# Optimization experiments

Hardware: AMD Instinct MI355X
Metric: run time of the kernel (lower is better)

Reference implementation:

```python
import jax, jax.numpy as jnp
import numpy as np

N, E, D, S, H, L = 20000, 320000, 128, 16, 4, 64


def _ln(x, g, b):
    m = x.mean(-1, keepdims=True)
    v = jnp.mean((x - m) ** 2, -1, keepdims=True)
    return (x - m) / jnp.sqrt(v + 1e-6) * g + b


def _mlp3(x, w1, b1, g1, be1, w2, b2, g2, be2, w3, b3):
    h = jax.nn.silu(_ln(x @ w1 + b1, g1, be1))
    h = jax.nn.silu(_ln(h @ w2 + b2, g2, be2))
    return h @ w3 + b3


def _seg_softmax(a, idx, n):
    # torch_geometric.utils.softmax: per-destination-group stable softmax
    m = jax.ops.segment_max(a, idx, num_segments=n)
    m = jnp.where(jnp.isfinite(m), m, 0.0)
    e = jnp.exp(a - m[idx])
    s = jax.ops.segment_sum(e, idx, num_segments=n)
    return e / (s[idx] + 1e-16)


def setup_inputs() -> dict:
    key = jax.random.key(0)
    ks = jax.random.split(key, 32)
    rn = lambda k, sh, sc=1.0: jax.random.normal(k, sh, dtype=jnp.float32) * sc
    li = lambda k, fi, fo: rn(k, (fi, fo), 1.0 / np.sqrt(fi))
    z = lambda n_: jnp.zeros((n_,), jnp.float32)
    o = lambda n_: jnp.ones((n_,), jnp.float32)
    inp = {
        'node_in': rn(ks[0], (N, D)),
        'node_embed': rn(ks[1], (N, D)),
        'edge_sh': rn(ks[2], (E, S)),
        'edge_length_embedding': rn(ks[3], (E, L)),
        'edge_src': jax.random.randint(ks[4], (E,), 0, N, dtype=jnp.int32),
        'edge_dst': jax.random.randint(ks[5], (E,), 0, N, dtype=jnp.int32),
        'batch': jnp.zeros((N,), jnp.int32),
        'pre_lin_w': li(ks[6], 2 * D + L, D),
        'tp2_w1': li(ks[7], L, 64), 'tp2_b1': z(64),
        'tp2_w2': li(ks[8], 64, H * S), 'tp2_b2': z(H * S),
        'a_w1': li(ks[9], L, 64), 'a_b1': z(64), 'a_g1': o(64), 'a_be1': z(64),
        'a_w2': li(ks[10], 64, 64), 'a_b2': z(64), 'a_g2': o(64), 'a_be2': z(64),
        'a_w3': li(ks[11], 64, H), 'a_b3': z(H),
        'lin_w': li(ks[12], D * H, D),
        'lin_edge_w': li(ks[13], D * H, 64),
        's_w1': li(ks[14], 64, 64), 's_b1': z(64), 's_g1': o(64), 's_be1': z(64),
        's_w2': li(ks[15], 64, 64), 's_b2': z(64), 's_g2': o(64), 's_be2': z(64),
        's_w3': li(ks[16], 64, 32), 's_b3': z(32),
    }
    return inp


def reference(node_in, node_embed, edge_sh, edge_length_embedding, edge_src, edge_dst, batch,
              pre_lin_w, tp2_w1, tp2_b1, tp2_w2, tp2_b2,
              a_w1, a_b1, a_g1, a_be1, a_w2, a_b2, a_g2, a_be2, a_w3, a_b3,
              lin_w, lin_edge_w,
              s_w1, s_b1, s_g1, s_be1, s_w2, s_b2, s_g2, s_be2, s_w3, s_b3):
    e = edge_length_embedding.shape[0]
    n = node_in.shape[0]
    # gather + pre_lin
    msg = jnp.concatenate([node_in[edge_src], node_in[edge_dst], edge_length_embedding], -1) @ pre_lin_w  # [E,D]
    # EquiConv tp2: channelwise TP with radial-MLP per-edge per-(head,sh) weights
    radial = jax.nn.silu(edge_length_embedding @ tp2_w1 + tp2_b1) @ tp2_w2 + tp2_b2  # [E,H*S]
    scal = jnp.einsum('ehs,es->eh', radial.reshape(e, H, S), edge_sh)  # [E,H]
    value = msg[:, None, :] * scal[:, :, None]  # [E,H,D]
    alpha = _mlp3(edge_length_embedding, a_w1, a_b1, a_g1, a_be1, a_w2, a_b2, a_g2, a_be2, a_w3, a_b3)  # [E,H]
    edge_out = value * alpha[:, :, None]  # [E,H,D]
    edge_scalar = _mlp3(edge_out.reshape(e, -1) @ lin_edge_w,
                        s_w1, s_b1, s_g1, s_be1, s_w2, s_b2, s_g2, s_be2, s_w3, s_b3)  # [E,32]
    asm = _seg_softmax(alpha, edge_dst, n)  # [E,H]
    node_fea = jax.ops.segment_sum(value * asm[:, :, None], edge_dst, num_segments=n)  # [N,H,D]
    node_out = node_fea.reshape(n, -1) @ lin_w  # [N,D]
    return node_out, edge_scalar
```

## Files before the change

kernel.cpp:

```cpp
#include <hip/hip_runtime.h>

#define NN 20000
#define EE 320000
#define WTOT 27648
#define P3N (EE*64/8 + NN*128/8)

typedef unsigned short u16;
typedef unsigned int u32;
typedef __attribute__((ext_vector_type(8))) short bf16x8;
typedef __attribute__((ext_vector_type(8))) _Float16 f16x8;
typedef __attribute__((ext_vector_type(4))) float f32x4;

__device__ __forceinline__ float bf2f(u16 u){
  union { u32 i; float f; } v; v.i = ((u32)u) << 16; return v.f;
}
__device__ __forceinline__ u16 f2bf(float f){
  union { float f; u32 i; } v; v.f = f;
  u32 i = v.i;
  return (u16)((i + 0x7FFFu + ((i >> 16) & 1u)) >> 16);
}
__device__ __forceinline__ u16 f2h(float f){
  union { _Float16 h[2]; u32 u; } v; v.h[0] = (_Float16)f;
  return (u16)(v.u & 0xFFFF);
}
__device__ __forceinline__ float h2f(u16 u){
  union { u32 i; _Float16 h[2]; } v; v.i = u; return (float)v.h[0];
}
__device__ __forceinline__ u32 packh2(float a, float b){
  return ((u32)f2h(b) << 16) | (u32)f2h(a);
}
__device__ __forceinline__ float fsilu(float y){
  return y * __builtin_amdgcn_rcpf(1.f + __expf(-y));
}

__global__ __launch_bounds__(256) void k_prep_all(
    const float* __restrict__ elen, const float* __restrict__ node_in,
    u16* __restrict__ elen16, u16* __restrict__ node16,
    int* __restrict__ counts,
    const float* __restrict__ plw, const float* __restrict__ lew,
    const float* __restrict__ lw,
    u16* __restrict__ Bt1, u16* __restrict__ Bt2, u16* __restrict__ Bt3,
    const float* __restrict__ aw1, const float* __restrict__ aw2, const float* __restrict__ aw3,
    const float* __restrict__ rw1, const float* __restrict__ rw2,
    const float* __restrict__ sw1, const float* __restrict__ sw2, const float* __restrict__ sw3,
    u16* __restrict__ W)
{
  size_t gi = (size_t)blockIdx.x * 256 + threadIdx.x;
  if (gi < (size_t)P3N) {
    const size_t n1 = (size_t)EE * 64 / 8;
    const float* src;
    u16* dst;
    if (gi < n1) { src = elen + gi*8; dst = elen16 + gi*8; }
    else { size_t j = gi - n1; src = node_in + j*8; dst = node16 + j*8; }
    float4 a = ((const float4*)src)[0];
    float4 b = ((const float4*)src)[1];
    uint4 vh;
    vh.x = packh2(a.x, a.y); vh.y = packh2(a.z, a.w);
    vh.z = packh2(b.x, b.y); vh.w = packh2(b.z, b.w);
    *(uint4*)dst = vh;
    return;
  }
  long j = (long)gi - P3N;
  if (j < NN) { counts[j] = 0; return; }
  j -= NN;
  if (j < 128*320) {
    int n = (int)j / 320, k = (int)j % 320;
    Bt1[j] = f2h(plw[k*128 + n]);
    return;
  }
  j -= 128*320;
  if (j < 256*128) {
    int n = (int)j / 128, k = (int)j % 128;
    int h = n >> 6, c = n & 63;
    Bt2[j] = f2h(lew[(h*128 + k)*64 + c]);
    return;
  }
  j -= 256*128;
  if (j < 128*512) {
    int n = (int)j / 512, k = (int)j % 512;
    Bt3[j] = f2bf(lw[k*128 + n]);
    return;
  }
  j -= 128*512;
  if (j < WTOT) {
    float v = 0.f;
    long i = j;
    if (i < 8192)      { int n = i >> 6, k = i & 63;
                         v = (n < 64) ? aw1[k*64 + n] : rw1[k*64 + (n - 64)]; }
    else if ((i -= 8192) < 4096) { int n = i >> 6, k = i & 63; v = aw2[k*64 + n]; }
    else if ((i -= 4096) < 1024) { int n = i >> 6, k = i & 63; v = (n < 4) ? aw3[k*4 + n] : 0.f; }
    else if ((i -= 1024) < 4096) { int n = i >> 6, k = i & 63; v = rw2[k*64 + n]; }
    else if ((i -= 4096) < 4096) { int n = i >> 6, k = i & 63; v = sw1[k*64 + n]; }
    else if ((i -= 4096) < 4096) { int n = i >> 6, k = i & 63; v = sw2[k*64 + n]; }
    else               { i -= 4096; int n = i >> 6, k = i & 63; v = sw3[k*32 + n]; }
    W[j] = f2h(v);
  }
}

__global__ __launch_bounds__(256) void k_count(const int* __restrict__ edst, int* __restrict__ counts){
  int e = blockIdx.x * 256 + threadIdx.x;
  if (e < EE) atomicAdd(&counts[edst[e]], 1);
}
__global__ __launch_bounds__(1024) void k_scan(const int* __restrict__ counts,
                                               int* __restrict__ offs, int* __restrict__ cursor){
  __shared__ int part[1024];
  int t = threadIdx.x;
  int c0 = t * 20, c1 = c0 + 20; if (c1 > NN) c1 = NN; if (c0 > NN) c0 = NN;
  int s = 0;
  for (int i = c0; i < c1; ++i) s += counts[i];
  part[t] = s;
  __syncthreads();
  int acc = s;
  #pragma unroll
  for (int d = 1; d < 1024; d <<= 1) {
    int v = (t >= d) ? part[t - d] : 0;
    __syncthreads();
    acc += v;
    part[t] = acc;
    __syncthreads();
  }
  if (t == 1023) offs[NN] = acc;
  int run = acc - s;
  for (int i = c0; i < c1; ++i) { offs[i] = run; cursor[i] = run; run += counts[i]; }
}
__global__ __launch_bounds__(256) void k_fill(const int* __restrict__ edst,
                                              int* __restrict__ cursor, int* __restrict__ eids){
  int e = blockIdx.x * 256 + threadIdx.x;
  if (e < EE) { int p = atomicAdd(&cursor[edst[e]], 1); eids[p] = e; }
}
__global__ __launch_bounds__(256) void k_sort2(const int* __restrict__ offs, int* __restrict__ eids){
  int w = threadIdx.x >> 6, lane = threadIdx.x & 63;
  int n = blockIdx.x * 4 + w;
  if (n >= NN) return;
  int beg = offs[n], end = offs[n+1], deg = end - beg;
  if (deg <= 1) return;
  if (deg <= 64) {
    int v = (lane < deg) ? eids[beg + lane] : 0x7fffffff;
    int rank = 0;
    for (int j = 0; j < deg; ++j) {
      int u = __shfl(v, j);
      rank += (u < v) ? 1 : 0;
    }
    if (lane < deg) eids[beg + rank] = v;
  } else if (lane == 0) {
    for (int i = beg + 1; i < end; ++i) {
      int v = eids[i]; int j = i - 1;
      while (j >= beg && eids[j] > v) { eids[j+1] = eids[j]; --j; }
      eids[j+1] = v;
    }
  }
}

template<int NI>
__device__ __forceinline__ void gemm16_lds(const u16 (*X)[72], int wrow, int lane,
                                           const u16* __restrict__ B, f32x4 acc[2][4])
{
  const int fr = lane & 15, fc = lane >> 4;
  #pragma unroll
  for (int mi = 0; mi < 2; ++mi)
    #pragma unroll
    for (int ni = 0; ni < NI; ++ni)
      acc[mi][ni] = (f32x4){0.f, 0.f, 0.f, 0.f};
  #pragma unroll
  for (int kk = 0; kk < 2; ++kk) {
    f16x8 a0 = *(const f16x8*)&X[wrow + fr][kk*32 + fc*8];
    f16x8 a1 = *(const f16x8*)&X[wrow + 16 + fr][kk*32 + fc*8];
    #pragma unroll
    for (int ni = 0; ni < NI; ++ni) {
      f16x8 b = *(const f16x8*)(B + (size_t)(ni*16 + fr)*64 + kk*32 + fc*8);
      acc[0][ni] = __builtin_amdgcn_mfma_f32_16x16x32_f16(a0, b, acc[0][ni], 0, 0, 0);
      acc[1][ni] = __builtin_amdgcn_mfma_f32_16x16x32_f16(a1, b, acc[1][ni], 0, 0, 0);
    }
  }
}

template<int NI>
__device__ __forceinline__ void gemm16_lds1(const u16 (*X)[72], int wrow, int lane,
                                            const u16* __restrict__ B, f32x4 acc[4])
{
  const int fr = lane & 15, fc = lane >> 4;
  #pragma unroll
  for (int ni = 0; ni < NI; ++ni) acc[ni] = (f32x4){0.f, 0.f, 0.f, 0.f};
  #pragma unroll
  for (int kk = 0; kk < 2; ++kk) {
    f16x8 a = *(const f16x8*)&X[wrow + fr][kk*32 + fc*8];
    #pragma unroll
    for (int ni = 0; ni < NI; ++ni) {
      f16x8 b = *(const f16x8*)(B + (size_t)(ni*16 + fr)*64 + kk*32 + fc*8);
      acc[ni] = __builtin_amdgcn_mfma_f32_16x16x32_f16(a, b, acc[ni], 0, 0, 0);
    }
  }
}

__device__ __forceinline__ void gemm16_glb8(const u16* __restrict__ X, int row0, int lane,
                                            const u16* __restrict__ B, f32x4 acc[2][8])
{
  const int fr = lane & 15, fc = lane >> 4;
  #pragma unroll
  for (int mi = 0; mi < 2; ++mi)
    #pragma unroll
    for (int ni = 0; ni < 8; ++ni)
      acc[mi][ni] = (f32x4){0.f, 0.f, 0.f, 0.f};
  #pragma unroll
  for (int kk = 0; kk < 2; ++kk) {
    f16x8 a0 = *(const f16x8*)(X + (size_t)(row0 + fr)*64 + kk*32 + fc*8);
    f16x8 a1 = *(const f16x8*)(X + (size_t)(row0 + 16 + fr)*64 + kk*32 + fc*8);
    #pragma unroll
    for (int ni = 0; ni < 8; ++ni) {
      f16x8 b = *(const f16x8*)(B + (size_t)(ni*16 + fr)*64 + kk*32 + fc*8);
      acc[0][ni] = __builtin_amdgcn_mfma_f32_16x16x32_f16(a0, b, acc[0][ni], 0, 0, 0);
      acc[1][ni] = __builtin_amdgcn_mfma_f32_16x16x32_f16(a1, b, acc[1][ni], 0, 0, 0);
    }
  }
}

template<bool LN>
__device__ __forceinline__ void act_store16(f32x4 acc[2][4],
    const float* __restrict__ b, const float* __restrict__ g, const float* __restrict__ be,
    u16 (*H)[72], int wrow, int lane)
{
  const int fr = lane & 15, fc = lane >> 4;
  float bv[4], gv[4], bev[4];
  #pragma unroll
  for (int ni = 0; ni < 4; ++ni) {
    bv[ni] = b[ni*16 + fr];
    if (LN) { gv[ni] = g[ni*16 + fr]; bev[ni] = be[ni*16 + fr]; }
  }
  #pragma unroll
  for (int mi = 0; mi < 2; ++mi)
    #pragma unroll
    for (int j = 0; j < 4; ++j) {
      int r = wrow + mi*16 + fc*4 + j;
      float x[4];
      #pragma unroll
      for (int ni = 0; ni < 4; ++ni) x[ni] = acc[mi][ni][j] + bv[ni];
      if (LN) {
        float s  = x[0] + x[1] + x[2] + x[3];
        float s2 = x[0]*x[0] + x[1]*x[1] + x[2]*x[2] + x[3]*x[3];
        #pragma unroll
        for (int off = 1; off < 16; off <<= 1) {
          s  += __shfl_xor(s,  off);
          s2 += __shfl_xor(s2, off);
        }
        float mu  = s * (1.f/64.f);
        float var = s2 * (1.f/64.f) - mu*mu;
        float rs  = rsqrtf(var + 1e-6f);
        #pragma unroll
        for (int ni = 0; ni < 4; ++ni) x[ni] = (x[ni] - mu)*rs*gv[ni] + bev[ni];
      }
      #pragma unroll
      for (int ni = 0; ni < 4; ++ni)
        H[r][ni*16 + fr] = f2h(fsilu(x[ni]));
    }
}

template<bool LN>
__device__ __forceinline__ void act_store16_1(f32x4 acc[4],
    const float* __restrict__ b, const float* __restrict__ g, const float* __restrict__ be,
    u16 (*H)[72], int wrow, int lane)
{
  const int fr = lane & 15, fc = lane >> 4;
  float bv[4], gv[4], bev[4];
  #pragma unroll
  for (int ni = 0; ni < 4; ++ni) {
    bv[ni] = b[ni*16 + fr];
    if (LN) { gv[ni] = g[ni*16 + fr]; bev[ni] = be[ni*16 + fr]; }
  }
  #pragma unroll
  for (int j = 0; j < 4; ++j) {
    int r = wrow + fc*4 + j;
    float x[4];
    #pragma unroll
    for (int ni = 0; ni < 4; ++ni) x[ni] = acc[ni][j] + bv[ni];
    if (LN) {
      float s  = x[0] + x[1] + x[2] + x[3];
      float s2 = x[0]*x[0] + x[1]*x[1] + x[2]*x[2] + x[3]*x[3];
      #pragma unroll
      for (int off = 1; off < 16; off <<= 1) {
        s  += __shfl_xor(s,  off);
        s2 += __shfl_xor(s2, off);
      }
      float mu  = s * (1.f/64.f);
      float var = s2 * (1.f/64.f) - mu*mu;
      float rs  = rsqrtf(var + 1e-6f);
      #pragma unroll
      for (int ni = 0; ni < 4; ++ni) x[ni] = (x[ni] - mu)*rs*gv[ni] + bev[ni];
    }
    #pragma unroll
    for (int ni = 0; ni < 4; ++ni)
      H[r][ni*16 + fr] = f2h(fsilu(x[ni]));
  }
}

union ESmem {
  struct { u16 Ha[128][72]; u16 Hr[128][72]; } m;
  struct { u16 As[128][40]; u16 Bs[128][40]; } g;
};
__global__ __launch_bounds__(256, 4) void k_edge1(
  const u16* __restrict__ elen16, const float* __restrict__ esh,
  const u16* __restrict__ Wm,
  const float* __restrict__ ab1, const float* __restrict__ ag1, const float* __restrict__ abe1,
  const float* __restrict__ ab2, const float* __restrict__ ag2, const float* __restrict__ abe2,
  const float* __restrict__ ab3,
  const float* __restrict__ tb1, const float* __restrict__ tb2,
  float* __restrict__ alpha_g, float* __restrict__ scal_g, float* __restrict__ cbuf_g,
  const u16* __restrict__ node16,
  const int* __restrict__ esrc, const int* __restrict__ edst,
  const u16* __restrict__ Bt1, u16* __restrict__ msgb)
{
  __shared__ ESmem u;
  __shared__ float aS[128][4];
  const u16* Wc1 = Wm;
  const u16* Wa2 = Wm + 8192;
  const u16* Wa3 = Wm + 12288;
  const u16* Wr2 = Wm + 13312;
  const int tid = threadIdx.x;
  const int wave = tid >> 6, lane = tid & 63;
  const int fr = lane & 15, fc = lane >> 4;
  const int e0 = blockIdx.x * 128;
  {
    const int wrow = wave * 32;
    {
      f32x4 acc8[2][8];
      gemm16_glb8(elen16, e0 + wrow, lane, Wc1, acc8);
      float bva[4], gva[4], beva[4], bvr[4];
      #pragma unroll
      for (int ni = 0; ni < 4; ++ni) {
        bva[ni] = ab1[ni*16 + fr]; gva[ni] = ag1[ni*16 + fr]; beva[ni] = abe1[ni*16 + fr];
        bvr[ni] = tb1[ni*16 + fr];
      }
      #pragma unroll
      for (int mi = 0; mi < 2; ++mi)
        #pragma unroll
        for (int j = 0; j < 4; ++j) {
          int r = wrow + mi*16 + fc*4 + j;
          float xa[4], xr[4];
          #pragma unroll
          for (int ni = 0; ni < 4; ++ni) {
            xa[ni] = acc8[mi][ni][j] + bva[ni];
            xr[ni] = acc8[mi][ni+4][j] + bvr[ni];
          }
          float s  = xa[0] + xa[1] + xa[2] + xa[3];
          float s2 = xa[0]*xa[0] + xa[1]*xa[1] + xa[2]*xa[2] + xa[3]*xa[3];
          #pragma unroll
          for (int off = 1; off < 16; off <<= 1) {
            s  += __shfl_xor(s,  off);
            s2 += __shfl_xor(s2, off);
          }
          float mu  = s * (1.f/64.f);
          float var = s2 * (1.f/64.f) - mu*mu;
          float rs  = rsqrtf(var + 1e-6f);
          #pragma unroll
          for (int ni = 0; ni < 4; ++ni) {
            float y = (xa[ni] - mu)*rs*gva[ni] + beva[ni];
            u.m.Ha[r][ni*16 + fr] = f2h(fsilu(y));
            u.m.Hr[r][ni*16 + fr] = f2h(fsilu(xr[ni]));
          }
        }
    }
    f32x4 acc[2][4];
    gemm16_lds<4>(u.m.Ha, wrow, lane, Wa2, acc);
    act_store16<true>(acc, ab2, ag2, abe2, u.m.Ha, wrow, lane);
    gemm16_lds<1>(u.m.Ha, wrow, lane, Wa3, acc);
    {
      float bv = (fr < 4) ? ab3[fr] : 0.f;
      #pragma unroll
      for (int mi = 0; mi < 2; ++mi)
        #pragma unroll
        for (int j = 0; j < 4; ++j) {
          int r = wrow + mi*16 + fc*4 + j;
          float v = acc[mi][0][j] + bv;
          if (fr < 4) {
            alpha_g[(size_t)(e0 + r)*4 + fr] = v;
            aS[r][fr] = v;
          }
        }
    }
    gemm16_lds<4>(u.m.Hr, wrow, lane, Wr2, acc);
    {
      float bv[4];
      #pragma unroll
      for (int ni = 0; ni < 4; ++ni) bv[ni] = tb2[ni*16 + fr];
      #pragma unroll
      for (int mi = 0; mi < 2; ++mi)
        #pragma unroll
        for (int j = 0; j < 4; ++j) {
          int r = wrow + mi*16 + fc*4 + j;
          float shv = esh[(size_t)(e0 + r)*16 + fr];
          float sc[4];
          #pragma unroll
          for (int ni = 0; ni < 4; ++ni) {
            float t = (acc[mi][ni][j] + bv[ni]) * shv;
            #pragma unroll
            for (int off = 1; off < 16; off <<= 1) t += __shfl_xor(t, off);
            sc[ni] = t;
          }
          if (fr == 0) {
            float4 sv; sv.x = sc[0]; sv.y = sc[1]; sv.z = sc[2]; sv.w = sc[3];
            *(float4*)(scal_g + (size_t)(e0 + r)*4) = sv;
            float4 cv;
            cv.x = sc[0]*aS[r][0]; cv.y = sc[1]*aS[r][1];
            cv.z = sc[2]*aS[r][2]; cv.w = sc[3]*aS[r][3];
            *(float4*)(cbuf_g + (size_t)(e0 + r)*4) = cv;
          }
        }
    }
  }
  __syncthreads();
  {
    const int wr = (wave >> 1) * 64, wc = (wave & 1) * 64;
    f32x4 acc[4][4] = {};
    const int r = tid >> 1, half = tid & 1;
    const int e = e0 + r;
    const int s_idx = esrc[e], d_idx = edst[e];
    for (int k0 = 0; k0 < 320; k0 += 32) {
      const int kk = k0 + half * 16;
      const u16* ap;
      if (kk < 128)      ap = node16 + (size_t)s_idx*128 + kk;
      else if (kk < 256) ap = node16 + (size_t)d_idx*128 + (kk - 128);
      else               ap = elen16 + (size_t)e*64 + (kk - 256);
      uint4* asp = (uint4*)&u.g.As[r][half*16];
      asp[0] = ((const uint4*)ap)[0];
      asp[1] = ((const uint4*)ap)[1];
      const uint4* bp = (const uint4*)(Bt1 + (size_t)r*320 + kk);
      *(uint4*)&u.g.Bs[r][half*16]     = bp[0];
      *(uint4*)&u.g.Bs[r][half*16 + 8] = bp[1];
      __syncthreads();
      f16x8 a[4], b[4];
      #pragma unroll
      for (int mi = 0; mi < 4; ++mi) a[mi] = *(const f16x8*)&u.g.As[wr + mi*16 + fr][fc*8];
      #pragma unroll
      for (int ni = 0; ni < 4; ++ni) b[ni] = *(const f16x8*)&u.g.Bs[wc + ni*16 + fr][fc*8];
      #pragma unroll
      for (int mi = 0; mi < 4; ++mi)
        #pragma unroll
        for (int ni = 0; ni < 4; ++ni)
          acc[mi][ni] = __builtin_amdgcn_mfma_f32_16x16x32_f16(a[mi], b[ni], acc[mi][ni], 0, 0, 0);
      __syncthreads();
    }
    #pragma unroll
    for (int mi = 0; mi < 4; ++mi)
      #pragma unroll
      for (int j = 0; j < 4; ++j) {
        int row = wr + mi*16 + fc*4 + j;
        size_t base = (size_t)(e0 + row)*128 + wc + fr;
        #pragma unroll
        for (int ni = 0; ni < 4; ++ni)
          msgb[base + ni*16] = f2h(acc[mi][ni][j]);
      }
  }
}

__global__ __launch_bounds__(256, 4) void g2s(
    const u16* __restrict__ msgb, const u16* __restrict__ Bt2,
    const float* __restrict__ cbuf, const u16* __restrict__ Wm,
    const float* __restrict__ b1, const float* __restrict__ g1, const float* __restrict__ be1,
    const float* __restrict__ b2, const float* __restrict__ g2, const float* __restrict__ be2,
    const float* __restrict__ b3,
    float* __restrict__ oute)
{
  __shared__ u16 Bs[256][40];
  __shared__ u16 X[64][72];
  __shared__ float cS[64][4];
  const u16* Ws1 = Wm + 17408;
  const u16* Ws2 = Wm + 21504;
  const u16* Ws3 = Wm + 25600;
  const int tid = threadIdx.x, wave = tid >> 6, lane = tid & 63;
  const int e0 = blockIdx.x * 64;
  const int fr = lane & 15, fc = lane >> 4;
  const int wrow = wave * 16;
  cS[tid >> 2][tid & 3] = cbuf[(size_t)e0*4 + tid];
  f16x8 a[4];
  {
    const u16* arow = msgb + (size_t)(e0 + wrow + fr)*128 + fc*8;
    #pragma unroll
    for (int k0i = 0; k0i < 4; ++k0i) a[k0i] = *(const f16x8*)(arow + k0i*32);
  }
  f32x4 acc[16];
  #pragma unroll
  for (int ni = 0; ni < 16; ++ni) acc[ni] = (f32x4){0.f, 0.f, 0.f, 0.f};
  const u16* bsrc = Bt2 + (size_t)tid*128;
  #pragma unroll
  for (int k0i = 0; k0i < 4; ++k0i) {
    {
      const uint4* bp = (const uint4*)(bsrc + k0i*32);
      *(uint4*)&Bs[tid][0]  = bp[0];
      *(uint4*)&Bs[tid][8]  = bp[1];
      *(uint4*)&Bs[tid][16] = bp[2];
      *(uint4*)&Bs[tid][24] = bp[3];
    }
    __syncthreads();
    #pragma unroll
    for (int ni = 0; ni < 16; ++ni) {
      f16x8 b = *(const f16x8*)&Bs[ni*16 + fr][fc*8];
      acc[ni] = __builtin_amdgcn_mfma_f32_16x16x32_f16(a[k0i], b, acc[ni], 0, 0, 0);
    }
    __syncthreads();
  }
  #pragma unroll
  for (int j = 0; j < 4; ++j) {
    int r = wrow + fc*4 + j;
    float c0 = cS[r][0], c1 = cS[r][1], c2 = cS[r][2], c3 = cS[r][3];
    #pragma unroll
    for (int m = 0; m < 4; ++m) {
      float y = c0*acc[m][j] + c1*acc[4+m][j] + c2*acc[8+m][j] + c3*acc[12+m][j];
      X[r][m*16 + fr] = f2h(y);
    }
  }
  f32x4 sa[4];
  gemm16_lds1<4>(X, wrow, lane, Ws1, sa);
  act_store16_1<true>(sa, b1, g1, be1, X, wrow, lane);
  gemm16_lds1<4>(X, wrow, lane, Ws2, sa);
  act_store16_1<true>(sa, b2, g2, be2, X, wrow, lane);
  gemm16_lds1<2>(X, wrow, lane, Ws3, sa);
  {
    float bv0 = b3[fr], bv1 = b3[16 + fr];
    #pragma unroll
    for (int j = 0; j < 4; ++j) {
      int r = wrow + fc*4 + j;
      oute[(size_t)(e0 + r)*32 + fr]      = sa[0][j] + bv0;
      oute[(size_t)(e0 + r)*32 + 16 + fr] = sa[1][j] + bv1;
    }
  }
}

__global__ __launch_bounds__(256) void k_node(
  const int* __restrict__ offs, const int* __restrict__ eids,
  const float* __restrict__ alpha, const float* __restrict__ scal,
  const u16* __restrict__ msgb, u16* __restrict__ nfb)
{
  const int w = threadIdx.x >> 6, lane = threadIdx.x & 63;
  const int n = blockIdx.x * 4 + w;
  const int beg = offs[n], end = offs[n+1];
  float m0=-3e38f, m1=-3e38f, m2=-3e38f, m3=-3e38f;
  for (int i = beg + lane; i < end; i += 64) {
    int eid = eids[i];
    float4 a = *(const float4*)(alpha + (size_t)eid*4);
    m0 = fmaxf(m0, a.x); m1 = fmaxf(m1, a.y);
    m2 = fmaxf(m2, a.z); m3 = fmaxf(m3, a.w);
  }
  #pragma unroll
  for (int off = 1; off < 64; off <<= 1) {
    m0 = fmaxf(m0, __shfl_xor(m0, off));
    m1 = fmaxf(m1, __shfl_xor(m1, off));
    m2 = fmaxf(m2, __shfl_xor(m2, off));
    m3 = fmaxf(m3, __shfl_xor(m3, off));
  }
  float se0=0.f, se1=0.f, se2=0.f, se3=0.f;
  float f00=0.f, f01=0.f, f10=0.f, f11=0.f, f20=0.f, f21=0.f, f30=0.f, f31=0.f;
  for (int i = beg; i < end; ++i) {
    int eid = eids[i];
    float4 a = *(const float4*)(alpha + (size_t)eid*4);
    float4 s = *(const float4*)(scal + (size_t)eid*4);
    float e0 = __expf(a.x - m0), e1 = __expf(a.y - m1);
    float e2 = __expf(a.z - m2), e3 = __expf(a.w - m3);
    se0 += e0; se1 += e1; se2 += e2; se3 += e3;
    float w0 = e0*s.x, w1 = e1*s.y, w2 = e2*s.z, w3 = e3*s.w;
    float v0 = h2f(msgb[(size_t)eid*128 + lane]);
    float v1 = h2f(msgb[(size_t)eid*128 + 64 + lane]);
    f00 = fmaf(w0, v0, f00); f01 = fmaf(w0, v1, f01);
    f10 = fmaf(w1, v0, f10); f11 = fmaf(w1, v1, f11);
    f20 = fmaf(w2, v0, f20); f21 = fmaf(w2, v1, f21);
    f30 = fmaf(w3, v0, f30); f31 = fmaf(w3, v1, f31);
  }
  float i0 = 1.f/(se0 + 1e-16f), i1 = 1.f/(se1 + 1e-16f);
  float i2 = 1.f/(se2 + 1e-16f), i3 = 1.f/(se3 + 1e-16f);
  size_t b = (size_t)n * 512;
  nfb[b + 0*128 + lane]      = f2bf(f00*i0);
  nfb[b + 0*128 + 64 + lane] = f2bf(f01*i0);
  nfb[b + 1*128 + lane]      = f2bf(f10*i1);
  nfb[b + 1*128 + 64 + lane] = f2bf(f11*i1);
  nfb[b + 2*128 + lane]      = f2bf(f20*i2);
  nfb[b + 2*128 + 64 + lane] = f2bf(f21*i2);
  nfb[b + 3*128 + lane]      = f2bf(f30*i3);
  nfb[b + 3*128 + 64 + lane] = f2bf(f31*i3);
}

__global__ __launch_bounds__(256) void g10_out(
    const u16* __restrict__ nfb, const u16* __restrict__ Bt3,
    float* __restrict__ out)
{
  __shared__ u16 As[128][40];
  __shared__ u16 Bs[128][40];
  const int tid = threadIdx.x;
  const int n0 = blockIdx.x * 128;
  const int wave = tid >> 6, lane = tid & 63;
  const int wr = (wave >> 1) * 64, wc = (wave & 1) * 64;
  const int fr = lane & 15, fc = lane >> 4;
  f32x4 acc[4][4] = {};
  const int r = tid >> 1, half = tid & 1;
  const int n = n0 + r;
  for (int k0 = 0; k0 < 512; k0 += 32) {
    uint4 z; z.x=0; z.y=0; z.z=0; z.w=0;
    uint4 v0 = z, v1 = z;
    if (n < NN) {
      const uint4* apv = (const uint4*)(nfb + (size_t)n*512 + k0 + half*16);
      v0 = apv[0]; v1 = apv[1];
    }
    *(uint4*)&As[r][half*16]     = v0;
    *(uint4*)&As[r][half*16 + 8] = v1;
    const uint4* bp = (const uint4*)(Bt3 + (size_t)r*512 + k0 + half*16);
    *(uint4*)&Bs[r][half*16]     = bp[0];
    *(uint4*)&Bs[r][half*16 + 8] = bp[1];
    __syncthreads();
    bf16x8 a[4], b[4];
    #pragma unroll
    for (int mi = 0; mi < 4; ++mi) a[mi] = *(const bf16x8*)&As[wr + mi*16 + fr][fc*8];
    #pragma unroll
    for (int ni = 0; ni < 4; ++ni) b[ni] = *(const bf16x8*)&Bs[wc + ni*16 + fr][fc*8];
    #pragma unroll
    for (int mi = 0; mi < 4; ++mi)
      #pragma unroll
      for (int ni = 0; ni < 4; ++ni)
        acc[mi][ni] = __builtin_amdgcn_mfma_f32_16x16x32_bf16(a[mi], b[ni], acc[mi][ni], 0, 0, 0);
    __syncthreads();
  }
  #pragma unroll
  for (int mi = 0; mi < 4; ++mi)
    #pragma unroll
    for (int j = 0; j < 4; ++j) {
      int rowg = n0 + wr + mi*16 + fc*4 + j;
      if (rowg < NN) {
        size_t base = (size_t)rowg*128 + wc + fr;
        #pragma unroll
        for (int ni = 0; ni < 4; ++ni)
          out[base + ni*16] = acc[mi][ni][j];
      }
    }
}

extern "C" void kernel_launch(void* const* d_in, const int* in_sizes, int n_in,
                              void* d_out, int out_size, void* d_ws, size_t ws_size,
                              hipStream_t stream)
{
  const float* node_in    = (const float*)d_in[0];
  const float* edge_sh    = (const float*)d_in[2];
  const float* elen       = (const float*)d_in[3];
  const int*   esrc       = (const int*)d_in[4];
  const int*   edst       = (const int*)d_in[5];
  const float* pre_lin_w  = (const float*)d_in[7];
  const float* tp2_w1     = (const float*)d_in[8];
  const float* tp2_b1     = (const float*)d_in[9];
  const float* tp2_w2     = (const float*)d_in[10];
  const float* tp2_b2     = (const float*)d_in[11];
  const float* a_w1  = (const float*)d_in[12];
  const float* a_b1  = (const float*)d_in[13];
  const float* a_g1  = (const float*)d_in[14];
  const float* a_be1 = (const float*)d_in[15];
  const float* a_w2  = (const float*)d_in[16];
  const float* a_b2  = (const float*)d_in[17];
  const float* a_g2  = (const float*)d_in[18];
  const float* a_be2 = (const float*)d_in[19];
  const float* a_w3  = (const float*)d_in[20];
  const float* a_b3  = (const float*)d_in[21];
  const float* lin_w      = (const float*)d_in[22];
  const float* lin_edge_w = (const float*)d_in[23];
  const float* s_w1  = (const float*)d_in[24];
  const float* s_b1  = (const float*)d_in[25];
  const float* s_g1  = (const float*)d_in[26];
  const float* s_be1 = (const float*)d_in[27];
  const float* s_w2  = (const float*)d_in[28];
  const float* s_b2  = (const float*)d_in[29];
  const float* s_g2  = (const float*)d_in[30];
  const float* s_be2 = (const float*)d_in[31];
  const float* s_w3  = (const float*)d_in[32];
  const float* s_b3  = (const float*)d_in[33];

  float* out_node = (float*)d_out;
  float* out_edge = out_node + (size_t)NN * 128;

  char* ws = (char*)d_ws;
  size_t off = 0;
  auto take = [&](size_t bytes) -> char* {
    char* p = ws + off;
    off = (off + bytes + 255) & ~(size_t)255;
    return p;
  };
  u16*   msgb   = (u16*)take((size_t)EE * 128 * 2);
  u16*   elen16 = (u16*)take((size_t)EE * 64 * 2);
  u16*   node16 = (u16*)take((size_t)NN * 128 * 2);
  u16*   nfb    = (u16*)take((size_t)NN * 512 * 2);
  float* alpha  = (float*)take((size_t)EE * 4 * 4);
  float* scal   = (float*)take((size_t)EE * 4 * 4);
  float* cbuf   = (float*)take((size_t)EE * 4 * 4);
  int*   counts = (int*)take((size_t)NN * 4);
  int*   offs   = (int*)take((size_t)(NN + 1) * 4);
  int*   cursor = (int*)take((size_t)NN * 4);
  int*   eids   = (int*)take((size_t)EE * 4);
  u16*   Bt1    = (u16*)take((size_t)128 * 320 * 2);
  u16*   Bt2    = (u16*)take((size_t)256 * 128 * 2);
  u16*   Bt3    = (u16*)take((size_t)128 * 512 * 2);
  u16*   Wmlp   = (u16*)take((size_t)WTOT * 2);

  const long prep_total = (long)P3N + NN + 128*320 + 256*128 + 128*512 + WTOT;
  k_prep_all<<<(int)((prep_total + 255)/256), 256, 0, stream>>>(
      elen, node_in, elen16, node16, counts,
      pre_lin_w, lin_edge_w, lin_w, Bt1, Bt2, Bt3,
      a_w1, a_w2, a_w3, tp2_w1, tp2_w2, s_w1, s_w2, s_w3, Wmlp);
  k_count<<<EE/256, 256, 0, stream>>>(edst, counts);
  k_scan<<<1, 1024, 0, stream>>>(counts, offs, cursor);
  k_fill<<<EE/256, 256, 0, stream>>>(edst, cursor, eids);
  k_sort2<<<NN/4, 256, 0, stream>>>(offs, eids);
  k_edge1<<<EE/128, 256, 0, stream>>>(elen16, edge_sh, Wmlp,
                                      a_b1, a_g1, a_be1, a_b2, a_g2, a_be2, a_b3,
                                      tp2_b1, tp2_b2, alpha, scal, cbuf,
                                      node16, esrc, edst, Bt1, msgb);
  g2s<<<EE/64, 256, 0, stream>>>(msgb, Bt2, cbuf, Wmlp,
                                 s_b1, s_g1, s_be1, s_b2, s_g2, s_be2, s_b3, out_edge);
  k_node<<<NN/4, 256, 0, stream>>>(offs, eids, alpha, scal, msgb, nfb);
  g10_out<<<(NN + 127)/128, 256, 0, stream>>>(nfb, Bt3, out_node);
}
```

Before: 400.1 us.

## Load gathered A operands directly into registers and double-buffer B tiles in pre_lin GEMM

The pre_lin gather-GEMM in k_edge1 no longer stages the gathered node/edge rows in shared memory. Each wave now owns 32 rows across all 128 output columns and loads its A fragments straight from global memory into registers. The B (weight) tiles are double-buffered in LDS so the next k-slice loads while the current one computes, leaving one barrier per iteration instead of two. The cost is more accumulator registers per thread (2x8 fragments) and uncoalesced 16-byte global gathers per lane, which may add latency at 4 blocks/SM occupancy.

```diff
diff --git a/kernel.cpp b/kernel.cpp
--- a/kernel.cpp
+++ b/kernel.cpp
@@ -294,7 +294,7 @@
 
 union ESmem {
   struct { u16 Ha[128][72]; u16 Hr[128][72]; } m;
-  struct { u16 As[128][40]; u16 Bs[128][40]; } g;
+  struct { u16 Bs[2][128][40]; } g;
 };
 __global__ __launch_bounds__(256, 4) void k_edge1(
   const u16* __restrict__ elen16, const float* __restrict__ esh,
@@ -317,9 +317,9 @@
   const int tid = threadIdx.x;
   const int wave = tid >> 6, lane = tid & 63;
   const int fr = lane & 15, fc = lane >> 4;
+  const int wrow = wave * 32;
   const int e0 = blockIdx.x * 128;
   {
-    const int wrow = wave * 32;
     {
       f32x4 acc8[2][8];
       gemm16_glb8(elen16, e0 + wrow, lane, Wc1, acc8);
@@ -408,44 +408,58 @@
   }
   __syncthreads();
   {
-    const int wr = (wave >> 1) * 64, wc = (wave & 1) * 64;
-    f32x4 acc[4][4] = {};
-    const int r = tid >> 1, half = tid & 1;
-    const int e = e0 + r;
-    const int s_idx = esrc[e], d_idx = edst[e];
-    for (int k0 = 0; k0 < 320; k0 += 32) {
-      const int kk = k0 + half * 16;
-      const u16* ap;
-      if (kk < 128)      ap = node16 + (size_t)s_idx*128 + kk;
-      else if (kk < 256) ap = node16 + (size_t)d_idx*128 + (kk - 128);
-      else               ap = elen16 + (size_t)e*64 + (kk - 256);
-      uint4* asp = (uint4*)&u.g.As[r][half*16];
-      asp[0] = ((const uint4*)ap)[0];
-      asp[1] = ((const uint4*)ap)[1];
-      const uint4* bp = (const uint4*)(Bt1 + (size_t)r*320 + kk);
-      *(uint4*)&u.g.Bs[r][half*16]     = bp[0];
-      *(uint4*)&u.g.Bs[r][half*16 + 8] = bp[1];
+    const int r0 = e0 + wrow + fr;
+    const int r1 = r0 + 16;
+    const int s0 = esrc[r0], d0 = edst[r0];
+    const int s1 = esrc[r1], d1 = edst[r1];
+    const int sr = tid >> 1, sh = tid & 1;
+    const u16* bstg = Bt1 + (size_t)sr*320 + sh*16;
+    {
+      const uint4* bp = (const uint4*)(bstg);
+      *(uint4*)&u.g.Bs[0][sr][sh*16]     = bp[0];
+      *(uint4*)&u.g.Bs[0][sr][sh*16 + 8] = bp[1];
+    }
+    f32x4 acc[2][8];
+    #pragma unroll
+    for (int mi = 0; mi < 2; ++mi)
+      #pragma unroll
+      for (int ni = 0; ni < 8; ++ni)
+        acc[mi][ni] = (f32x4){0.f, 0.f, 0.f, 0.f};
+    __syncthreads();
+    #pragma unroll
+    for (int k0i = 0; k0i < 10; ++k0i) {
+      const int buf = k0i & 1;
+      if (k0i + 1 < 10) {
+        const uint4* bp = (const uint4*)(bstg + (k0i + 1)*32);
+        *(uint4*)&u.g.Bs[buf^1][sr][sh*16]     = bp[0];
+        *(uint4*)&u.g.Bs[buf^1][sr][sh*16 + 8] = bp[1];
+      }
+      const int k0 = k0i * 32;
+      const u16 *ap0, *ap1;
+      if (k0 < 128)      { ap0 = node16 + (size_t)s0*128 + k0;
+                           ap1 = node16 + (size_t)s1*128 + k0; }
+      else if (k0 < 256) { ap0 = node16 + (size_t)d0*128 + (k0 - 128);
+                           ap1 = node16 + (size_t)d1*128 + (k0 - 128); }
+      else               { ap0 = elen16 + (size_t)r0*64 + (k0 - 256);
+                           ap1 = elen16 + (size_t)r1*64 + (k0 - 256); }
+      f16x8 a0 = *(const f16x8*)(ap0 + fc*8);
+      f16x8 a1 = *(const f16x8*)(ap1 + fc*8);
+      #pragma unroll
+      for (int ni = 0; ni < 8; ++ni) {
+        f16x8 b = *(const f16x8*)&u.g.Bs[buf][ni*16 + fr][fc*8];
+        acc[0][ni] = __builtin_amdgcn_mfma_f32_16x16x32_f16(a0, b, acc[0][ni], 0, 0, 0);
+        acc[1][ni] = __builtin_amdgcn_mfma_f32_16x16x32_f16(a1, b, acc[1][ni], 0, 0, 0);
+      }
       __syncthreads();
-      f16x8 a[4], b[4];
-      #pragma unroll
-      for (int mi = 0; mi < 4; ++mi) a[mi] = *(const f16x8*)&u.g.As[wr + mi*16 + fr][fc*8];
-      #pragma unroll
-      for (int ni = 0; ni < 4; ++ni) b[ni] = *(const f16x8*)&u.g.Bs[wc + ni*16 + fr][fc*8];
-      #pragma unroll
-      for (int mi = 0; mi < 4; ++mi)
+    }
+    #pragma unroll
+    for (int mi = 0; mi < 2; ++mi)
+      #pragma unroll
+      for (int j = 0; j < 4; ++j) {
+        int row = wrow + mi*16 + fc*4 + j;
+        size_t base = (size_t)(e0 + row)*128 + fr;
         #pragma unroll
-        for (int ni = 0; ni < 4; ++ni)
-          acc[mi][ni] = __builtin_amdgcn_mfma_f32_16x16x32_f16(a[mi], b[ni], acc[mi][ni], 0, 0, 0);
-      __syncthreads();
-    }
-    #pragma unroll
-    for (int mi = 0; mi < 4; ++mi)
-      #pragma unroll
-      for (int j = 0; j < 4; ++j) {
-        int row = wr + mi*16 + fc*4 + j;
-        size_t base = (size_t)(e0 + row)*128 + wc + fr;
-        #pragma unroll
-        for (int ni = 0; ni < 4; ++ni)
+        for (int ni = 0; ni < 8; ++ni)
           msgb[base + ni*16] = f2h(acc[mi][ni][j]);
       }
   }
```

After: 401.7 us. Within noise of the previous version (+0.4%).
